# Performance work log

Measured on AMD Instinct MI355X. Metric: run time of the kernel, lower is better.

## Reference

```python
import jax, jax.numpy as jnp
import numpy as np
from jax import lax

D_MODEL = 1024
D_FF = 4096
K = 5
PAD = K // 2


def setup_inputs() -> dict:
    key = jax.random.key(0)
    ks = jax.random.split(key, 12)
    s_in = 1.0 / np.sqrt(D_MODEL)
    s_ff = 1.0 / np.sqrt(D_FF)
    s_k = 1.0 / np.sqrt(K)  # depthwise conv fan_in = 1*K
    return {
        "x": jax.random.normal(ks[0], (4, 2048, D_MODEL), dtype=jnp.float32),
        "Wg": jax.random.uniform(ks[1], (D_MODEL, D_FF), jnp.float32, -s_in, s_in),
        "bg": jax.random.uniform(ks[2], (D_FF,), jnp.float32, -s_in, s_in),
        "Wu": jax.random.uniform(ks[3], (D_MODEL, D_FF), jnp.float32, -s_in, s_in),
        "bu": jax.random.uniform(ks[4], (D_FF,), jnp.float32, -s_in, s_in),
        "convg_w": jax.random.uniform(ks[5], (D_FF, 1, K), jnp.float32, -s_k, s_k),
        "convg_b": jax.random.uniform(ks[6], (D_FF,), jnp.float32, -s_k, s_k),
        "convu_w": jax.random.uniform(ks[7], (D_FF, 1, K), jnp.float32, -s_k, s_k),
        "convu_b": jax.random.uniform(ks[8], (D_FF,), jnp.float32, -s_k, s_k),
        "Wd": jax.random.uniform(ks[9], (D_FF, D_MODEL), jnp.float32, -s_ff, s_ff),
        "bd": jax.random.uniform(ks[10], (D_MODEL,), jnp.float32, -s_ff, s_ff),
    }


def _dwconv(h, w, b):
    # h: [B, L, C] -> depthwise conv along L with 'same' padding -> [B, L, C]
    y = lax.conv_general_dilated(
        h.transpose(0, 2, 1),  # [B, C, L]
        w,                      # [C, 1, K]
        window_strides=(1,),
        padding=[(PAD, PAD)],
        feature_group_count=h.shape[-1],
    )
    return (y + b[None, :, None]).transpose(0, 2, 1)


def reference(x, Wg, bg, Wu, bu, convg_w, convg_b, convu_w, convu_b, Wd, bd):
    gate = _dwconv(jnp.einsum("bld,df->blf", x, Wg) + bg, convg_w, convg_b)
    up = _dwconv(jnp.einsum("bld,df->blf", x, Wu) + bu, convu_w, convu_b)
    h = jax.nn.silu(gate) * up
    return jnp.einsum("blf,fd->bld", h, Wd) + bd
```

## Files before the change

### kernel.cpp

```cpp
#include <hip/hip_runtime.h>
#include <hip/hip_bf16.h>
#include <cstdint>

#define BATCH  4
#define SEQ    2048
#define DMODEL 1024
#define DFF    4096
#define MTOT   (BATCH * SEQ)
#define KCONV  5
#define PADC   2

using bf16raw = unsigned short;
typedef __attribute__((ext_vector_type(8))) short bf16x8;
typedef __attribute__((ext_vector_type(4))) float f32x4;

__device__ __forceinline__ float bf2f(bf16raw u) {
    return __uint_as_float(((uint32_t)u) << 16);
}
__device__ __forceinline__ bf16raw f2bf(float f) {
    uint32_t u = __float_as_uint(f);
    u = (u + 0x7fffu + ((u >> 16) & 1u)) >> 16;
    return (bf16raw)u;
}


__global__ __launch_bounds__(256)
void cvt_bf16_kernel(const float* __restrict__ in, bf16raw* __restrict__ out, int n4)
{
    const int i = blockIdx.x * 256 + threadIdx.x;
    if (i >= n4) return;
    const float4 v = reinterpret_cast<const float4*>(in)[i];
    ushort4 o;
    o.x = f2bf(v.x); o.y = f2bf(v.y); o.z = f2bf(v.z); o.w = f2bf(v.w);
    reinterpret_cast<ushort4*>(out)[i] = o;
}

__global__ __launch_bounds__(256)
void transpose_cvt_kernel(const float* __restrict__ in, bf16raw* __restrict__ out,
                          int R, int C)
{
    __shared__ float tile[32][33];
    const int r0 = blockIdx.y * 32, c0 = blockIdx.x * 32;
    const int tx = threadIdx.x & 31, ty = threadIdx.x >> 5;
#pragma unroll
    for (int i = 0; i < 4; ++i)
        tile[ty + i * 8][tx] = in[(size_t)(r0 + ty + i * 8) * C + c0 + tx];
    __syncthreads();
#pragma unroll
    for (int i = 0; i < 4; ++i)
        out[(size_t)(c0 + ty + i * 8) * R + r0 + tx] = f2bf(tile[tx][ty + i * 8]);
}

__global__ __launch_bounds__(256)
void convw_reorder_kernel(const float* __restrict__ wg, const float* __restrict__ wu,
                          float* __restrict__ wgT, float* __restrict__ wuT)
{
    const int i = blockIdx.x * 256 + threadIdx.x;
    if (i >= KCONV * DFF) return;
    const int j = i / DFF, f = i - j * DFF;
    wgT[i] = wg[f * KCONV + j];
    wuT[i] = wu[f * KCONV + j];
}


__device__ __forceinline__ void gll16(const bf16raw* g, const char* lds)
{
    __builtin_amdgcn_global_load_lds(
        (const __attribute__((address_space(1))) void*)g,
        (__attribute__((address_space(3))) void*)lds, 16, 0, 0);
}

template<typename CT, bool BIAS, int SPLITK>
__global__ __launch_bounds__(512, 2)
void gemm256_kernel(const bf16raw* __restrict__ A, const bf16raw* __restrict__ BT,
                    const float* __restrict__ bias0, const float* __restrict__ bias1,
                    CT* __restrict__ C, int M, int N, int K, int nbm, int nbn)
{
    __shared__ __align__(16) char smem[131072];

    const int tid  = threadIdx.x;
    const int lane = tid & 63;
    const int wave = __builtin_amdgcn_readfirstlane(tid >> 6);
    const int wr = wave >> 2;
    const int wc = wave & 3;

    const int nwg = nbm * nbn * SPLITK;
    const int cpx = nwg >> 3;
    const int bid = blockIdx.x;
    const int swz = (bid & 7) * cpx + (bid >> 3);
    int sk = 0, rem = swz;
    if constexpr (SPLITK > 1) { sk = swz / (nbm * nbn); rem = swz - sk * (nbm * nbn); }
    const int bx = rem / nbm;
    const int by = rem - bx * nbm;
    const int bm = by * 256;
    const int bn = bx * 256;

    const int klen = K / SPLITK;
    const int kbeg = sk * klen;
    const int NT   = klen / 64;
    CT* Cp = C + (size_t)sk * M * N;

    const int srow = tid >> 3;
    const int kswz = (((tid & 7) ^ ((tid >> 3) & 7)) << 3);
    const bf16raw* Asrc = A  + (size_t)(bm + srow) * K + kbeg + kswz;
    const bf16raw* Bsrc = BT + (size_t)(bn + srow) * K + kbeg + kswz;

    const int g4  = lane >> 4;
    const int r15 = lane & 15;
    const int key = lane & 7;
    const int off0 = r15 * 128 + (((0 + g4) ^ key) << 4);
    const int off1 = r15 * 128 + (((4 + g4) ^ key) << 4);

    f32x4 acc[8][4];
#pragma unroll
    for (int i = 0; i < 8; ++i)
#pragma unroll
        for (int j = 0; j < 4; ++j) acc[i][j] = (f32x4){0.f, 0.f, 0.f, 0.f};

    auto stage = [&](int t, int buf) {
        const bf16raw* Ag = Asrc + (size_t)t * 64;
        const bf16raw* Bg = Bsrc + (size_t)t * 64;
        const char* la = smem + buf * 65536 + tid * 16;
        const char* lb = la + 32768;
#pragma unroll
        for (int i = 0; i < 4; ++i) {
            gll16(Ag + (size_t)i * 64 * K, la + i * 8192);
            gll16(Bg + (size_t)i * 64 * K, lb + i * 8192);
        }
    };

    auto compute = [&](int buf) {
        const char* bufA = smem + buf * 65536 + wr * 16384;
        const char* bufB = smem + buf * 65536 + 32768 + wc * 8192;
        bf16x8 bfr[4][2];
#pragma unroll
        for (int nf = 0; nf < 4; ++nf) {
            bfr[nf][0] = *(const bf16x8*)(bufB + nf * 2048 + off0);
            bfr[nf][1] = *(const bf16x8*)(bufB + nf * 2048 + off1);
        }
#pragma unroll
        for (int q = 0; q < 4; ++q) {
            bf16x8 afr[2][2];
#pragma unroll
            for (int m2 = 0; m2 < 2; ++m2) {
                afr[m2][0] = *(const bf16x8*)(bufA + (q * 2 + m2) * 2048 + off0);
                afr[m2][1] = *(const bf16x8*)(bufA + (q * 2 + m2) * 2048 + off1);
            }
            __builtin_amdgcn_s_setprio(1);
#pragma unroll
            for (int m2 = 0; m2 < 2; ++m2)
#pragma unroll
                for (int nf = 0; nf < 4; ++nf) {
                    acc[q * 2 + m2][nf] = __builtin_amdgcn_mfma_f32_16x16x32_bf16(
                        afr[m2][0], bfr[nf][0], acc[q * 2 + m2][nf], 0, 0, 0);
                    acc[q * 2 + m2][nf] = __builtin_amdgcn_mfma_f32_16x16x32_bf16(
                        afr[m2][1], bfr[nf][1], acc[q * 2 + m2][nf], 0, 0, 0);
                }
            __builtin_amdgcn_s_setprio(0);
        }
    };

    stage(0, 0);
    for (int t = 0; t < NT; ++t) {
        const int cur = t & 1;
        if (t + 1 < NT) {
            stage(t + 1, cur ^ 1);
            asm volatile("s_waitcnt vmcnt(8)" ::: "memory");
        } else {
            asm volatile("s_waitcnt vmcnt(0)" ::: "memory");
        }
        __builtin_amdgcn_s_barrier();
        compute(cur);
        __builtin_amdgcn_s_barrier();
        asm volatile("" ::: "memory");
    }

    const int er = g4 << 2;
#pragma unroll
    for (int nf = 0; nf < 4; ++nf) {
        const int nn = bn + wc * 64 + nf * 16 + r15;
        float bv = 0.f;
        if constexpr (BIAS) bv = (nn < DFF) ? bias0[nn] : bias1[nn - DFF];
#pragma unroll
        for (int mf = 0; mf < 8; ++mf) {
            const int mrow = bm + wr * 128 + mf * 16 + er;
#pragma unroll
            for (int j = 0; j < 4; ++j) {
                const float v = acc[mf][nf][j] + bv;
                if constexpr (sizeof(CT) == 2)
                    Cp[(size_t)(mrow + j) * N + nn] = f2bf(v);
                else
                    Cp[(size_t)(mrow + j) * N + nn] = v;
            }
        }
    }
}

__global__ __launch_bounds__(256)
void reduce_bias_kernel(const float* __restrict__ part, const float* __restrict__ bd,
                        float* __restrict__ out)
{
    const int i = blockIdx.x * 256 + threadIdx.x;
    const int d = (i & (DMODEL / 4 - 1)) * 4;
    const float4 a = reinterpret_cast<const float4*>(part)[i];
    const float4 b = reinterpret_cast<const float4*>(part + (size_t)MTOT * DMODEL)[i];
    const float4 bb = *reinterpret_cast<const float4*>(bd + d);
    float4 o;
    o.x = a.x + b.x + bb.x; o.y = a.y + b.y + bb.y;
    o.z = a.z + b.z + bb.z; o.w = a.w + b.w + bb.w;
    reinterpret_cast<float4*>(out)[i] = o;
}

__global__ __launch_bounds__(256)
void conv_silu_mul_bf16_kernel(const bf16raw* __restrict__ gp, const bf16raw* __restrict__ up,
                               const float* __restrict__ wgT, const float* __restrict__ cbg,
                               const float* __restrict__ wuT, const float* __restrict__ cbu,
                               bf16raw* __restrict__ h, int S)
{
    const int idx = blockIdx.x * 256 + threadIdx.x;
    const int f   = (idx & (DFF / 8 - 1)) << 3;
    const int row = idx >> 9;
    const int l   = row & (SEQ - 1);
    const int rb  = row - l;

    float g[8], u[8];
    {
        const float4 a0 = *reinterpret_cast<const float4*>(cbg + f);
        const float4 a1 = *reinterpret_cast<const float4*>(cbg + f + 4);
        const float4 b0 = *reinterpret_cast<const float4*>(cbu + f);
        const float4 b1 = *reinterpret_cast<const float4*>(cbu + f + 4);
        g[0]=a0.x; g[1]=a0.y; g[2]=a0.z; g[3]=a0.w; g[4]=a1.x; g[5]=a1.y; g[6]=a1.z; g[7]=a1.w;
        u[0]=b0.x; u[1]=b0.y; u[2]=b0.z; u[3]=b0.w; u[4]=b1.x; u[5]=b1.y; u[6]=b1.z; u[7]=b1.w;
    }

#pragma unroll
    for (int j = 0; j < KCONV; ++j) {
        const int ls = l + j - PADC;
        if (ls < 0 || ls >= SEQ) continue;
        const size_t off = (size_t)(rb + ls) * S + f;
        const bf16x8 gv = *reinterpret_cast<const bf16x8*>(gp + off);
        const bf16x8 uv = *reinterpret_cast<const bf16x8*>(up + off);
        const float4 wa0 = *reinterpret_cast<const float4*>(wgT + j * DFF + f);
        const float4 wa1 = *reinterpret_cast<const float4*>(wgT + j * DFF + f + 4);
        const float4 wb0 = *reinterpret_cast<const float4*>(wuT + j * DFF + f);
        const float4 wb1 = *reinterpret_cast<const float4*>(wuT + j * DFF + f + 4);
        const float wg8[8] = {wa0.x, wa0.y, wa0.z, wa0.w, wa1.x, wa1.y, wa1.z, wa1.w};
        const float wu8[8] = {wb0.x, wb0.y, wb0.z, wb0.w, wb1.x, wb1.y, wb1.z, wb1.w};
#pragma unroll
        for (int c = 0; c < 8; ++c) {
            g[c] += bf2f((bf16raw)gv[c]) * wg8[c];
            u[c] += bf2f((bf16raw)uv[c]) * wu8[c];
        }
    }

    bf16x8 hv;
#pragma unroll
    for (int c = 0; c < 8; ++c) {
        const float s = g[c] / (1.f + __expf(-g[c]));
        hv[c] = (short)f2bf(s * u[c]);
    }
    *reinterpret_cast<bf16x8*>(h + (size_t)row * DFF + f) = hv;
}


#define BM 128
#define BN 128
#define BK 8

__device__ __forceinline__ void load4f(const float* p, float v[4]) {
    const float4 t = *reinterpret_cast<const float4*>(p);
    v[0] = t.x; v[1] = t.y; v[2] = t.z; v[3] = t.w;
}

__global__ __launch_bounds__(256)
void sgemm_bias_kernel(const float* __restrict__ A, const float* __restrict__ B,
                       const float* __restrict__ bias, float* __restrict__ C,
                       int N, int K)
{
    __shared__ float As[BK][BM];
    __shared__ float Bs[BK][BN];

    const int tid = threadIdx.x;
    const int bm  = blockIdx.y * BM;
    const int bn  = blockIdx.x * BN;
    const int tx  = tid & 15;
    const int ty  = tid >> 4;

    const int arow = tid >> 1;
    const int acol = (tid & 1) * 4;
    const int brow = tid >> 5;
    const int bcol = (tid & 31) * 4;

    const float* Ap = A + (size_t)(bm + arow) * K + acol;
    const float* Bp = B + (size_t)brow * N + bn + bcol;

    float acc[8][8];
#pragma unroll
    for (int i = 0; i < 8; ++i)
#pragma unroll
        for (int j = 0; j < 8; ++j) acc[i][j] = 0.f;

    for (int k0 = 0; k0 < K; k0 += BK) {
        float av[4];
        load4f(Ap + k0, av);
        const float4 bv = *reinterpret_cast<const float4*>(Bp + (size_t)k0 * N);
        __syncthreads();
#pragma unroll
        for (int i = 0; i < 4; ++i) As[acol + i][arow] = av[i];
        *reinterpret_cast<float4*>(&Bs[brow][bcol]) = bv;
        __syncthreads();
#pragma unroll
        for (int kk = 0; kk < BK; ++kk) {
            const float4 a0 = *reinterpret_cast<const float4*>(&As[kk][ty * 4]);
            const float4 a1 = *reinterpret_cast<const float4*>(&As[kk][64 + ty * 4]);
            const float4 b0 = *reinterpret_cast<const float4*>(&Bs[kk][tx * 4]);
            const float4 b1 = *reinterpret_cast<const float4*>(&Bs[kk][64 + tx * 4]);
            const float am[8] = {a0.x, a0.y, a0.z, a0.w, a1.x, a1.y, a1.z, a1.w};
            const float bb[8] = {b0.x, b0.y, b0.z, b0.w, b1.x, b1.y, b1.z, b1.w};
#pragma unroll
            for (int mi = 0; mi < 8; ++mi)
#pragma unroll
                for (int nj = 0; nj < 8; ++nj)
                    acc[mi][nj] += am[mi] * bb[nj];
        }
    }
#pragma unroll
    for (int mi = 0; mi < 8; ++mi) {
        const int m = bm + ((mi < 4) ? (ty * 4 + mi) : (64 + ty * 4 + (mi - 4)));
#pragma unroll
        for (int g = 0; g < 2; ++g) {
            const int n = bn + g * 64 + tx * 4;
            float4 o;
            o.x = acc[mi][g * 4 + 0] + bias[n + 0];
            o.y = acc[mi][g * 4 + 1] + bias[n + 1];
            o.z = acc[mi][g * 4 + 2] + bias[n + 2];
            o.w = acc[mi][g * 4 + 3] + bias[n + 3];
            *reinterpret_cast<float4*>(&C[(size_t)m * N + n]) = o;
        }
    }
}

__global__ __launch_bounds__(256)
void conv_silu_mul_f32_kernel(const float* __restrict__ gp, const float* __restrict__ up,
                              const float* __restrict__ wg, const float* __restrict__ cbg,
                              const float* __restrict__ wu, const float* __restrict__ cbu,
                              float* __restrict__ hout)
{
    const int idx = blockIdx.x * 256 + threadIdx.x;
    const int f   = (idx & (DFF / 4 - 1)) * 4;
    const int l   = idx >> 10;

    float g[4], u[4];
    load4f(cbg + f, g);
    load4f(cbu + f, u);
#pragma unroll
    for (int j = 0; j < KCONV; ++j) {
        const int ls = l + j - PADC;
        if (ls < 0 || ls >= SEQ) continue;
        const size_t off = (size_t)ls * DFF + f;
        float gv[4], uv[4];
        load4f(gp + off, gv);
        load4f(up + off, uv);
#pragma unroll
        for (int c = 0; c < 4; ++c) {
            g[c] += gv[c] * wg[(f + c) * KCONV + j];
            u[c] += uv[c] * wu[(f + c) * KCONV + j];
        }
    }
    float h[4];
#pragma unroll
    for (int c = 0; c < 4; ++c) {
        const float s = g[c] / (1.f + __expf(-g[c]));
        h[c] = s * u[c];
    }
    float4 o; o.x = h[0]; o.y = h[1]; o.z = h[2]; o.w = h[3];
    *reinterpret_cast<float4*>(&hout[(size_t)l * DFF + f]) = o;
}


extern "C" void kernel_launch(void* const* d_in, const int* in_sizes, int n_in,
                              void* d_out, int out_size, void* d_ws, size_t ws_size,
                              hipStream_t stream)
{
    const float* x   = (const float*)d_in[0];
    const float* Wg  = (const float*)d_in[1];
    const float* bg  = (const float*)d_in[2];
    const float* Wu  = (const float*)d_in[3];
    const float* bu  = (const float*)d_in[4];
    const float* cgw = (const float*)d_in[5];
    const float* cgb = (const float*)d_in[6];
    const float* cuw = (const float*)d_in[7];
    const float* cub = (const float*)d_in[8];
    const float* Wd  = (const float*)d_in[9];
    const float* bd  = (const float*)d_in[10];
    float* out = (float*)d_out;

    const dim3 blk(256);
    auto align256 = [](size_t v) { return (v + 255) & ~(size_t)255; };

    const size_t SZ_XB  = (size_t)MTOT * DMODEL * 2;
    const size_t SZ_WGU = (size_t)2 * DFF * DMODEL * 2;
    const size_t SZ_WD  = (size_t)DMODEL * DFF * 2;
    const size_t SZ_CW  = (size_t)KCONV * DFF * 4;
    const size_t SZ_H   = (size_t)MTOT * DFF * 2;
    const size_t SZ_UP  = (size_t)MTOT * 2 * DFF * 2;

    size_t cur = 0;
    const size_t oXB  = cur; cur = align256(cur + SZ_XB);
    const size_t oWGU = cur; cur = align256(cur + SZ_WGU);
    const size_t oWD  = cur; cur = align256(cur + SZ_WD);
    const size_t oCWg = cur; cur = align256(cur + SZ_CW);
    const size_t oCWu = cur; cur = align256(cur + SZ_CW);
    const size_t oH   = cur; cur = align256(cur + SZ_H);
    const size_t oUP  = cur; cur = align256(cur + SZ_UP);
    const size_t need = cur;

    if (ws_size >= need) {
        bf16raw* xb   = (bf16raw*)((char*)d_ws + oXB);
        bf16raw* Wgu  = (bf16raw*)((char*)d_ws + oWGU);
        bf16raw* WdT  = (bf16raw*)((char*)d_ws + oWD);
        float*   cwg  = (float*)((char*)d_ws + oCWg);
        float*   cwu  = (float*)((char*)d_ws + oCWu);
        bf16raw* h    = (bf16raw*)((char*)d_ws + oH);
        bf16raw* Cup  = (bf16raw*)((char*)d_ws + oUP);
        float*   part = (float*)((char*)d_ws + oUP);

        cvt_bf16_kernel<<<(MTOT * DMODEL / 4 + 255) / 256, blk, 0, stream>>>(x, xb, MTOT * DMODEL / 4);
        transpose_cvt_kernel<<<dim3(DFF / 32, DMODEL / 32), blk, 0, stream>>>(Wg, Wgu, DMODEL, DFF);
        transpose_cvt_kernel<<<dim3(DFF / 32, DMODEL / 32), blk, 0, stream>>>(Wu, Wgu + (size_t)DFF * DMODEL, DMODEL, DFF);
        transpose_cvt_kernel<<<dim3(DMODEL / 32, DFF / 32), blk, 0, stream>>>(Wd, WdT, DFF, DMODEL);
        convw_reorder_kernel<<<(KCONV * DFF + 255) / 256, blk, 0, stream>>>(cgw, cuw, cwg, cwu);

        {
            const int nbm = MTOT / 256, nbn = (2 * DFF) / 256;
            gemm256_kernel<bf16raw, true, 1><<<nbm * nbn, dim3(512), 0, stream>>>(
                xb, Wgu, bg, bu, Cup, MTOT, 2 * DFF, DMODEL, nbm, nbn);
        }

        conv_silu_mul_bf16_kernel<<<MTOT * (DFF / 8) / 256, blk, 0, stream>>>(
            Cup, Cup + DFF, cwg, cgb, cwu, cub, h, 2 * DFF);

        {
            const int nbm = MTOT / 256, nbn = DMODEL / 256;
            gemm256_kernel<float, false, 2><<<nbm * nbn * 2, dim3(512), 0, stream>>>(
                h, WdT, nullptr, nullptr, part, MTOT, DMODEL, DFF, nbm, nbn);
        }
        reduce_bias_kernel<<<MTOT * DMODEL / 4 / 256, blk, 0, stream>>>(part, bd, out);
        return;
    }

    const size_t CE  = (size_t)SEQ * DFF;
    const size_t P32 = CE * sizeof(float);
    if (ws_size < 3 * P32) return;

    float* gpre = (float*)d_ws;
    float* upre = gpre + CE;
    float* hbuf = upre + CE;
    dim3 gu(DFF / BN, SEQ / BM);
    dim3 gdc(DMODEL / BN, SEQ / BM);
    const int nconv = SEQ * (DFF / 4) / 256;
    for (int b = 0; b < BATCH; ++b) {
        const float* xbp = x + (size_t)b * SEQ * DMODEL;
        float* outb = out + (size_t)b * SEQ * DMODEL;
        sgemm_bias_kernel<<<gu, blk, 0, stream>>>(xbp, Wg, bg, gpre, DFF, DMODEL);
        sgemm_bias_kernel<<<gu, blk, 0, stream>>>(xbp, Wu, bu, upre, DFF, DMODEL);
        conv_silu_mul_f32_kernel<<<nconv, blk, 0, stream>>>(gpre, upre, cgw, cgb, cuw, cub, hbuf);
        sgemm_bias_kernel<<<gdc, blk, 0, stream>>>(hbuf, Wd, bd, outb, DMODEL, DFF);
    }
}
```

Measured before the change: 386.2 us.

## Interleave global-to-LDS prefetch with MFMA phases in an 8-phase GEMM pipeline

Replaces the simple double-buffered stage/compute loop with a finer-grained schedule. Loads for tiles t+1 and t+2 are split into quarter chunks and issued between the four MFMA sub-phases, each separated by a barrier. A-tile rows are remapped so half of the next A tile can be prefetched while the current buffer is still being read. The goal is to hide global load latency and smooth memory issue across the compute loop. The cost is eight barriers per K step instead of two, plus more intricate vmcnt accounting, which could add stalls or cause a correctness hazard if the counts are wrong.

```diff
diff --git a/kernel.cpp b/kernel.cpp
--- a/kernel.cpp
+++ b/kernel.cpp
@@ -72,9 +72,9 @@
 
 template<typename CT, bool BIAS, int SPLITK>
 __global__ __launch_bounds__(512, 2)
-void gemm256_kernel(const bf16raw* __restrict__ A, const bf16raw* __restrict__ BT,
-                    const float* __restrict__ bias0, const float* __restrict__ bias1,
-                    CT* __restrict__ C, int M, int N, int K, int nbm, int nbn)
+void gemm8p_kernel(const bf16raw* __restrict__ A, const bf16raw* __restrict__ BT,
+                   const float* __restrict__ bias0, const float* __restrict__ bias1,
+                   CT* __restrict__ C, int M, int N, int K, int nbm, int nbn)
 {
     __shared__ __align__(16) char smem[131072];
 
@@ -100,16 +100,31 @@
     const int NT   = klen / 64;
     CT* Cp = C + (size_t)sk * M * N;
 
-    const int srow = tid >> 3;
-    const int kswz = (((tid & 7) ^ ((tid >> 3) & 7)) << 3);
-    const bf16raw* Asrc = A  + (size_t)(bm + srow) * K + kbeg + kswz;
-    const bf16raw* Bsrc = BT + (size_t)(bn + srow) * K + kbeg + kswz;
+    const int bchunk = tid & 7;
+    const int brow_l = tid >> 3;
+    const int ahalf  = tid >> 8;
+    const int arow32 = (tid & 255) >> 3;
+
+    auto stageB = [&](int t, int j) {
+        const int row = j * 64 + brow_l;
+        const bf16raw* src = BT + (size_t)(bn + row) * K + kbeg + t * 64
+                             + ((bchunk ^ (row & 7)) << 3);
+        const char* dst = smem + (t & 1) * 65536 + 32768 + j * 8192 + tid * 16;
+        gll16(src, dst);
+    };
+    auto stageA = [&](int t, int q) {
+        const int row = ahalf * 128 + q * 32 + arow32;
+        const bf16raw* src = A + (size_t)(bm + row) * K + kbeg + t * 64
+                             + ((bchunk ^ (row & 7)) << 3);
+        const char* dst = smem + (t & 1) * 65536 + row * 128 + bchunk * 16;
+        gll16(src, dst);
+    };
 
     const int g4  = lane >> 4;
     const int r15 = lane & 15;
     const int key = lane & 7;
-    const int off0 = r15 * 128 + (((0 + g4) ^ key) << 4);
-    const int off1 = r15 * 128 + (((4 + g4) ^ key) << 4);
+    const int sw0 = ((0 + g4) ^ key) << 4;
+    const int sw1 = ((4 + g4) ^ key) << 4;
 
     f32x4 acc[8][4];
 #pragma unroll
@@ -117,35 +132,46 @@
 #pragma unroll
         for (int j = 0; j < 4; ++j) acc[i][j] = (f32x4){0.f, 0.f, 0.f, 0.f};
 
-    auto stage = [&](int t, int buf) {
-        const bf16raw* Ag = Asrc + (size_t)t * 64;
-        const bf16raw* Bg = Bsrc + (size_t)t * 64;
-        const char* la = smem + buf * 65536 + tid * 16;
-        const char* lb = la + 32768;
-#pragma unroll
-        for (int i = 0; i < 4; ++i) {
-            gll16(Ag + (size_t)i * 64 * K, la + i * 8192);
-            gll16(Bg + (size_t)i * 64 * K, lb + i * 8192);
-        }
-    };
-
-    auto compute = [&](int buf) {
-        const char* bufA = smem + buf * 65536 + wr * 16384;
-        const char* bufB = smem + buf * 65536 + 32768 + wc * 8192;
+#pragma unroll
+    for (int j = 0; j < 4; ++j) stageB(0, j);
+#pragma unroll
+    for (int q = 0; q < 4; ++q) stageA(0, q);
+#pragma unroll
+    for (int j = 0; j < 4; ++j) stageB(1, j);
+    stageA(1, 0); stageA(1, 1);
+    asm volatile("s_waitcnt vmcnt(6)" ::: "memory");
+    __builtin_amdgcn_s_barrier();
+    asm volatile("" ::: "memory");
+
+    for (int t = 0; t < NT; ++t) {
+        const char* base = smem + (t & 1) * 65536;
         bf16x8 bfr[4][2];
 #pragma unroll
-        for (int nf = 0; nf < 4; ++nf) {
-            bfr[nf][0] = *(const bf16x8*)(bufB + nf * 2048 + off0);
-            bfr[nf][1] = *(const bf16x8*)(bufB + nf * 2048 + off1);
-        }
-#pragma unroll
         for (int q = 0; q < 4; ++q) {
+            if (q == 0) {
+#pragma unroll
+                for (int nf = 0; nf < 4; ++nf) {
+                    bfr[nf][0] = *(const bf16x8*)(base + 32768 + wc * 8192 + nf * 2048 + r15 * 128 + sw0);
+                    bfr[nf][1] = *(const bf16x8*)(base + 32768 + wc * 8192 + nf * 2048 + r15 * 128 + sw1);
+                }
+            }
             bf16x8 afr[2][2];
 #pragma unroll
             for (int m2 = 0; m2 < 2; ++m2) {
-                afr[m2][0] = *(const bf16x8*)(bufA + (q * 2 + m2) * 2048 + off0);
-                afr[m2][1] = *(const bf16x8*)(bufA + (q * 2 + m2) * 2048 + off1);
+                afr[m2][0] = *(const bf16x8*)(base + wr * 16384 + q * 4096 + m2 * 2048 + r15 * 128 + sw0);
+                afr[m2][1] = *(const bf16x8*)(base + wr * 16384 + q * 4096 + m2 * 2048 + r15 * 128 + sw1);
             }
+            if (q == 0)      { if (t + 1 < NT) { stageA(t + 1, 2); stageA(t + 1, 3); } }
+            else if (q == 1) { if (t + 2 < NT) { stageB(t + 2, 0); stageB(t + 2, 1); } }
+            else if (q == 2) { if (t + 2 < NT) { stageB(t + 2, 2); stageB(t + 2, 3); } }
+            else             { if (t + 2 < NT) { stageA(t + 2, 0); stageA(t + 2, 1); } }
+            if (q == 3) {
+                if (t + 2 < NT)      asm volatile("s_waitcnt vmcnt(6)" ::: "memory");
+                else if (t + 1 < NT) asm volatile("s_waitcnt vmcnt(0)" ::: "memory");
+            }
+            asm volatile("" ::: "memory");
+            __builtin_amdgcn_s_barrier();
+            asm volatile("" ::: "memory");
             __builtin_amdgcn_s_setprio(1);
 #pragma unroll
             for (int m2 = 0; m2 < 2; ++m2)
@@ -157,22 +183,10 @@
                         afr[m2][1], bfr[nf][1], acc[q * 2 + m2][nf], 0, 0, 0);
                 }
             __builtin_amdgcn_s_setprio(0);
-        }
-    };
-
-    stage(0, 0);
-    for (int t = 0; t < NT; ++t) {
-        const int cur = t & 1;
-        if (t + 1 < NT) {
-            stage(t + 1, cur ^ 1);
-            asm volatile("s_waitcnt vmcnt(8)" ::: "memory");
-        } else {
-            asm volatile("s_waitcnt vmcnt(0)" ::: "memory");
-        }
-        __builtin_amdgcn_s_barrier();
-        compute(cur);
-        __builtin_amdgcn_s_barrier();
-        asm volatile("" ::: "memory");
+            asm volatile("" ::: "memory");
+            __builtin_amdgcn_s_barrier();
+            asm volatile("" ::: "memory");
+        }
     }
 
     const int er = g4 << 2;
@@ -433,7 +447,7 @@
 
         {
             const int nbm = MTOT / 256, nbn = (2 * DFF) / 256;
-            gemm256_kernel<bf16raw, true, 1><<<nbm * nbn, dim3(512), 0, stream>>>(
+            gemm8p_kernel<bf16raw, true, 1><<<nbm * nbn, dim3(512), 0, stream>>>(
                 xb, Wgu, bg, bu, Cup, MTOT, 2 * DFF, DMODEL, nbm, nbn);
         }
 
@@ -442,7 +456,7 @@
 
         {
             const int nbm = MTOT / 256, nbn = DMODEL / 256;
-            gemm256_kernel<float, false, 2><<<nbm * nbn * 2, dim3(512), 0, stream>>>(
+            gemm8p_kernel<float, false, 2><<<nbm * nbn * 2, dim3(512), 0, stream>>>(
                 h, WdT, nullptr, nullptr, part, MTOT, DMODEL, DFF, nbm, nbn);
         }
         reduce_bias_kernel<<<MTOT * DMODEL / 4 / 256, blk, 0, stream>>>(part, bd, out);
```

Result: no change. 389.6 us (+0.9%).

## Halve GEMM K-tile to fit two blocks per CU, raise down-proj split-K

Applied to the files above, without the earlier changes.

The bf16 GEMM now stages 32-wide K slices instead of 64. This halves the double-buffered LDS footprint to 64KB, so two 512-thread workgroups can share a CU, and it uses a new XOR swizzle on 64-byte rows. The down-projection split-K goes from 2 to 4 to fill the GPU with more workgroups, and the reduction kernel is templated over the number of partials. In exchange there are twice as many barriers per K step and more fp32 partial-sum traffic written and re-read.

```diff
diff --git a/kernel.cpp b/kernel.cpp
--- a/kernel.cpp
+++ b/kernel.cpp
@@ -63,7 +63,7 @@
 }
 
 
-__device__ __forceinline__ void gll16(const bf16raw* g, const char* lds)
+__device__ __forceinline__ void gll16(const bf16raw* g, const bf16raw* lds)
 {
     __builtin_amdgcn_global_load_lds(
         (const __attribute__((address_space(1))) void*)g,
@@ -72,11 +72,11 @@
 
 template<typename CT, bool BIAS, int SPLITK>
 __global__ __launch_bounds__(512, 2)
-void gemm256_kernel(const bf16raw* __restrict__ A, const bf16raw* __restrict__ BT,
-                    const float* __restrict__ bias0, const float* __restrict__ bias1,
-                    CT* __restrict__ C, int M, int N, int K, int nbm, int nbn)
-{
-    __shared__ __align__(16) char smem[131072];
+void gemm2b_kernel(const bf16raw* __restrict__ A, const bf16raw* __restrict__ BT,
+                   const float* __restrict__ bias0, const float* __restrict__ bias1,
+                   CT* __restrict__ C, int M, int N, int K, int nbm, int nbn)
+{
+    __shared__ bf16raw smem[2][2][256 * 32];
 
     const int tid  = threadIdx.x;
     const int lane = tid & 63;
@@ -97,19 +97,31 @@
 
     const int klen = K / SPLITK;
     const int kbeg = sk * klen;
-    const int NT   = klen / 64;
+    const int NT   = klen / 32;
     CT* Cp = C + (size_t)sk * M * N;
 
-    const int srow = tid >> 3;
-    const int kswz = (((tid & 7) ^ ((tid >> 3) & 7)) << 3);
-    const bf16raw* Asrc = A  + (size_t)(bm + srow) * K + kbeg + kswz;
-    const bf16raw* Bsrc = BT + (size_t)(bn + srow) * K + kbeg + kswz;
+    const int srow   = tid >> 2;
+    const int schunk = tid & 3;
+
+    auto stage = [&](int t, int buf) {
+#pragma unroll
+        for (int u = 0; u < 2; ++u) {
+            const int ra = u * 128 + srow;
+            gll16(A + (size_t)(bm + ra) * K + kbeg + t * 32
+                    + ((schunk ^ ((ra >> 1) & 3)) << 3),
+                  &smem[buf][0][ra * 32 + schunk * 8]);
+        }
+#pragma unroll
+        for (int u = 0; u < 2; ++u) {
+            const int rb = u * 128 + srow;
+            gll16(BT + (size_t)(bn + rb) * K + kbeg + t * 32
+                    + ((schunk ^ ((rb >> 1) & 3)) << 3),
+                  &smem[buf][1][rb * 32 + schunk * 8]);
+        }
+    };
 
     const int g4  = lane >> 4;
     const int r15 = lane & 15;
-    const int key = lane & 7;
-    const int off0 = r15 * 128 + (((0 + g4) ^ key) << 4);
-    const int off1 = r15 * 128 + (((4 + g4) ^ key) << 4);
 
     f32x4 acc[8][4];
 #pragma unroll
@@ -117,62 +129,38 @@
 #pragma unroll
         for (int j = 0; j < 4; ++j) acc[i][j] = (f32x4){0.f, 0.f, 0.f, 0.f};
 
-    auto stage = [&](int t, int buf) {
-        const bf16raw* Ag = Asrc + (size_t)t * 64;
-        const bf16raw* Bg = Bsrc + (size_t)t * 64;
-        const char* la = smem + buf * 65536 + tid * 16;
-        const char* lb = la + 32768;
-#pragma unroll
-        for (int i = 0; i < 4; ++i) {
-            gll16(Ag + (size_t)i * 64 * K, la + i * 8192);
-            gll16(Bg + (size_t)i * 64 * K, lb + i * 8192);
-        }
-    };
-
     auto compute = [&](int buf) {
-        const char* bufA = smem + buf * 65536 + wr * 16384;
-        const char* bufB = smem + buf * 65536 + 32768 + wc * 8192;
-        bf16x8 bfr[4][2];
+        bf16x8 bfr[4];
 #pragma unroll
         for (int nf = 0; nf < 4; ++nf) {
-            bfr[nf][0] = *(const bf16x8*)(bufB + nf * 2048 + off0);
-            bfr[nf][1] = *(const bf16x8*)(bufB + nf * 2048 + off1);
-        }
-#pragma unroll
-        for (int q = 0; q < 4; ++q) {
-            bf16x8 afr[2][2];
-#pragma unroll
-            for (int m2 = 0; m2 < 2; ++m2) {
-                afr[m2][0] = *(const bf16x8*)(bufA + (q * 2 + m2) * 2048 + off0);
-                afr[m2][1] = *(const bf16x8*)(bufA + (q * 2 + m2) * 2048 + off1);
-            }
-            __builtin_amdgcn_s_setprio(1);
-#pragma unroll
-            for (int m2 = 0; m2 < 2; ++m2)
-#pragma unroll
-                for (int nf = 0; nf < 4; ++nf) {
-                    acc[q * 2 + m2][nf] = __builtin_amdgcn_mfma_f32_16x16x32_bf16(
-                        afr[m2][0], bfr[nf][0], acc[q * 2 + m2][nf], 0, 0, 0);
-                    acc[q * 2 + m2][nf] = __builtin_amdgcn_mfma_f32_16x16x32_bf16(
-                        afr[m2][1], bfr[nf][1], acc[q * 2 + m2][nf], 0, 0, 0);
-                }
-            __builtin_amdgcn_s_setprio(0);
-        }
+            const int row = wc * 64 + nf * 16 + r15;
+            bfr[nf] = *(const bf16x8*)&smem[buf][1][row * 32 + ((g4 ^ ((row >> 1) & 3)) << 3)];
+        }
+        __builtin_amdgcn_s_setprio(1);
+#pragma unroll
+        for (int mf = 0; mf < 8; ++mf) {
+            const int row = wr * 128 + mf * 16 + r15;
+            const bf16x8 a = *(const bf16x8*)&smem[buf][0][row * 32 + ((g4 ^ ((row >> 1) & 3)) << 3)];
+#pragma unroll
+            for (int nf = 0; nf < 4; ++nf)
+                acc[mf][nf] = __builtin_amdgcn_mfma_f32_16x16x32_bf16(
+                    a, bfr[nf], acc[mf][nf], 0, 0, 0);
+        }
+        __builtin_amdgcn_s_setprio(0);
     };
 
     stage(0, 0);
     for (int t = 0; t < NT; ++t) {
-        const int cur = t & 1;
+        const int buf = t & 1;
         if (t + 1 < NT) {
-            stage(t + 1, cur ^ 1);
-            asm volatile("s_waitcnt vmcnt(8)" ::: "memory");
+            stage(t + 1, buf ^ 1);
+            asm volatile("s_waitcnt vmcnt(4)" ::: "memory");
         } else {
             asm volatile("s_waitcnt vmcnt(0)" ::: "memory");
         }
         __builtin_amdgcn_s_barrier();
-        compute(cur);
+        compute(buf);
         __builtin_amdgcn_s_barrier();
-        asm volatile("" ::: "memory");
     }
 
     const int er = g4 << 2;
@@ -196,18 +184,20 @@
     }
 }
 
+template<int NS>
 __global__ __launch_bounds__(256)
 void reduce_bias_kernel(const float* __restrict__ part, const float* __restrict__ bd,
                         float* __restrict__ out)
 {
     const int i = blockIdx.x * 256 + threadIdx.x;
     const int d = (i & (DMODEL / 4 - 1)) * 4;
-    const float4 a = reinterpret_cast<const float4*>(part)[i];
-    const float4 b = reinterpret_cast<const float4*>(part + (size_t)MTOT * DMODEL)[i];
     const float4 bb = *reinterpret_cast<const float4*>(bd + d);
-    float4 o;
-    o.x = a.x + b.x + bb.x; o.y = a.y + b.y + bb.y;
-    o.z = a.z + b.z + bb.z; o.w = a.w + b.w + bb.w;
+    float4 o; o.x = bb.x; o.y = bb.y; o.z = bb.z; o.w = bb.w;
+#pragma unroll
+    for (int s = 0; s < NS; ++s) {
+        const float4 a = reinterpret_cast<const float4*>(part + (size_t)s * MTOT * DMODEL)[i];
+        o.x += a.x; o.y += a.y; o.z += a.z; o.w += a.w;
+    }
     reinterpret_cast<float4*>(out)[i] = o;
 }
 
@@ -433,7 +423,7 @@
 
         {
             const int nbm = MTOT / 256, nbn = (2 * DFF) / 256;
-            gemm256_kernel<bf16raw, true, 1><<<nbm * nbn, dim3(512), 0, stream>>>(
+            gemm2b_kernel<bf16raw, true, 1><<<nbm * nbn, dim3(512), 0, stream>>>(
                 xb, Wgu, bg, bu, Cup, MTOT, 2 * DFF, DMODEL, nbm, nbn);
         }
 
@@ -442,10 +432,10 @@
 
         {
             const int nbm = MTOT / 256, nbn = DMODEL / 256;
-            gemm256_kernel<float, false, 2><<<nbm * nbn * 2, dim3(512), 0, stream>>>(
+            gemm2b_kernel<float, false, 4><<<nbm * nbn * 4, dim3(512), 0, stream>>>(
                 h, WdT, nullptr, nullptr, part, MTOT, DMODEL, DFF, nbm, nbn);
         }
-        reduce_bias_kernel<<<MTOT * DMODEL / 4 / 256, blk, 0, stream>>>(part, bd, out);
+        reduce_bias_kernel<4><<<MTOT * DMODEL / 4 / 256, blk, 0, stream>>>(part, bd, out);
         return;
     }
 
```

After: 432.3 us. 11.9% more time.
